# Kernel optimization log

Hardware: AMD Instinct MI355X
Metric: run time of the kernel (lower is better)

Reference implementation:

```python
import jax, jax.numpy as jnp
import numpy as np
import math

EPS = 1e-5


def _layernorm(x, gamma, beta):
    mu = jnp.mean(x, axis=-1, keepdims=True)
    var = jnp.mean(jnp.square(x - mu), axis=-1, keepdims=True)
    return (x - mu) * jax.lax.rsqrt(var + EPS) * gamma + beta


def setup_inputs() -> dict:
    key = jax.random.key(0)
    ks = jax.random.split(key, 8)
    B, Sq, Sk, D = 2, 2048, 2048, 1024
    s = 1.0 / math.sqrt(D)
    return {
        "Q": jax.random.normal(ks[0], (B, Sq, D), jnp.float32),
        "K": jax.random.normal(ks[1], (B, Sk, D), jnp.float32),
        "Wq": jax.random.normal(ks[2], (D, D), jnp.float32) * s,
        "bq": jnp.zeros((D,), jnp.float32),
        "Wk": jax.random.normal(ks[3], (D, D), jnp.float32) * s,
        "bk": jnp.zeros((D,), jnp.float32),
        "Wv": jax.random.normal(ks[4], (D, D), jnp.float32) * s,
        "bv": jnp.zeros((D,), jnp.float32),
        "Wo": jax.random.normal(ks[5], (D, D), jnp.float32) * s,
        "bo": jnp.zeros((D,), jnp.float32),
        "g0": jnp.ones((D,), jnp.float32),
        "b0": jnp.zeros((D,), jnp.float32),
        "g1": jnp.ones((D,), jnp.float32),
        "b1": jnp.zeros((D,), jnp.float32),
    }


def reference(Q, K, Wq, bq, Wk, bk, Wv, bv, Wo, bo, g0, b0, g1, b1):
    H = 16
    B, Sq, D = Q.shape
    dh = D // H
    Qp = Q @ Wq + bq                      # [B,Sq,D]
    Kp = K @ Wk + bk                      # [B,Sk,D]
    # Faithful to source: fc_v is applied to the ALREADY-projected K
    Vp = Kp @ Wv + bv                     # [B,Sk,D]
    # split heads: [B,S,H,dh] -> [B,H,S,dh]
    Qh = Qp.reshape(B, Sq, H, dh).transpose(0, 2, 1, 3)
    Kh = Kp.reshape(B, -1, H, dh).transpose(0, 2, 1, 3)
    Vh = Vp.reshape(B, -1, H, dh).transpose(0, 2, 1, 3)
    scores = jnp.einsum("bhqd,bhkd->bhqk", Qh, Kh) / math.sqrt(dh)
    attn = jax.nn.softmax(scores, axis=-1)  # dropout is identity in eval mode
    Oh = Qh + jnp.einsum("bhqk,bhkd->bhqd", attn, Vh)
    O = Oh.transpose(0, 2, 1, 3).reshape(B, Sq, D)
    O = _layernorm(O, g0, b0)
    O = O + jax.nn.gelu(O @ Wo + bo, approximate=False)
    O = _layernorm(O, g1, b1)
    return O
```

## Files before the change

kernel.cpp:

```cpp
#include <hip/hip_runtime.h>
#include <hip/hip_bf16.h>

typedef __attribute__((ext_vector_type(8))) short short8;
typedef __attribute__((ext_vector_type(4))) float f32x4;
typedef __attribute__((ext_vector_type(8))) unsigned short ushort8;

__device__ __forceinline__ unsigned short f32_to_bf16(float f) {
  return __builtin_bit_cast(unsigned short, __float2bfloat16(f));
}
__device__ __forceinline__ float bf16_to_f32(unsigned short u) {
  return __builtin_bit_cast(float, (unsigned)u << 16);
}

__device__ __forceinline__ void gload_lds16(const unsigned short* g, unsigned short* l) {
  __builtin_amdgcn_global_load_lds((const __attribute__((address_space(1))) void*)g,
                                   (__attribute__((address_space(3))) void*)l, 16, 0, 0);
}

__global__ __launch_bounds__(256) void transpose4_kernel(const float* __restrict__ W0,
                                                         const float* __restrict__ W1,
                                                         const float* __restrict__ W2,
                                                         const float* __restrict__ W3,
                                                         unsigned short* __restrict__ T0,
                                                         unsigned short* __restrict__ T1,
                                                         unsigned short* __restrict__ T2,
                                                         unsigned short* __restrict__ T3) {
  __shared__ float t[32][33];
  const int D = 1024;
  const float* Ws[4] = {W0, W1, W2, W3};
  unsigned short* Ts[4] = {T0, T1, T2, T3};
  const float* W = Ws[blockIdx.z];
  unsigned short* WT = Ts[blockIdx.z];
  int bx = blockIdx.x, by = blockIdx.y;
  int tx = threadIdx.x, ty = threadIdx.y;
#pragma unroll
  for (int i = 0; i < 4; ++i)
    t[ty * 4 + i][tx] = W[(size_t)(by * 32 + ty * 4 + i) * D + bx * 32 + tx];
  __syncthreads();
#pragma unroll
  for (int i = 0; i < 4; ++i) {
    int r = ty * 4 + i;
    WT[(size_t)(bx * 32 + r) * D + by * 32 + tx] = f32_to_bf16(t[tx][r]);
  }
}

template <bool GELU_RES, bool A_F32>
__device__ __forceinline__ void gemm_body(const void* __restrict__ Av,
                                          const unsigned short* __restrict__ Bt,
                                          const float* __restrict__ bias,
                                          const unsigned short* __restrict__ res16,
                                          float* __restrict__ out32,
                                          unsigned short* __restrict__ out16,
                                          unsigned short* __restrict__ outT,
                                          float o16_scale,
                                          int M, int N, int K,
                                          unsigned short* As, unsigned short* Bs) {
  const int tid = threadIdx.x;
  const int lane = tid & 63, wid = tid >> 6;
  const int wm = wid >> 2, wn = wid & 3;
  const int m0 = blockIdx.x * 64, n0 = blockIdx.y * 128;
  const int lr = lane & 15, lg = lane >> 4;
  const int xs = lr & 7;
  f32x4 acc[2][2] = {};
  for (int kt = 0; kt < K; kt += 64) {
#pragma unroll
    for (int i = 0; i < 2; ++i) {
      int c = tid + i * 512;
      int r = c >> 3, pc = c & 7;
      int lc = pc ^ (r & 7);
      gload_lds16(Bt + (size_t)(n0 + r) * K + kt + lc * 8, Bs + c * 8);
    }
    {
      int c = tid;
      int r = c >> 3, pc = c & 7;
      int lc = pc ^ (r & 7);
      if (A_F32) {
        const float* src = (const float*)Av + (size_t)(m0 + r) * K + kt + lc * 8;
        float4 f0 = *(const float4*)(src);
        float4 f1 = *(const float4*)(src + 4);
        ushort8 o;
        o[0] = f32_to_bf16(f0.x); o[1] = f32_to_bf16(f0.y);
        o[2] = f32_to_bf16(f0.z); o[3] = f32_to_bf16(f0.w);
        o[4] = f32_to_bf16(f1.x); o[5] = f32_to_bf16(f1.y);
        o[6] = f32_to_bf16(f1.z); o[7] = f32_to_bf16(f1.w);
        *(ushort8*)(As + c * 8) = o;
      } else {
        gload_lds16((const unsigned short*)Av + (size_t)(m0 + r) * K + kt + lc * 8,
                    As + c * 8);
      }
    }
    __syncthreads();
#pragma unroll
    for (int ks = 0; ks < 2; ++ks) {
      short8 af[2], bfr[2];
#pragma unroll
      for (int mf = 0; mf < 2; ++mf)
        af[mf] = *(const short8*)(As + (wm * 32 + mf * 16 + lr) * 64 +
                                  (((ks * 4 + lg) ^ xs) << 3));
#pragma unroll
      for (int nf = 0; nf < 2; ++nf)
        bfr[nf] = *(const short8*)(Bs + (wn * 32 + nf * 16 + lr) * 64 +
                                   (((ks * 4 + lg) ^ xs) << 3));
#pragma unroll
      for (int mf = 0; mf < 2; ++mf)
#pragma unroll
        for (int nf = 0; nf < 2; ++nf)
          acc[mf][nf] = __builtin_amdgcn_mfma_f32_16x16x32_bf16(af[mf], bfr[nf], acc[mf][nf], 0, 0, 0);
    }
    __syncthreads();
  }
#pragma unroll
  for (int nf = 0; nf < 2; ++nf) {
    int cn = n0 + wn * 32 + nf * 16 + lr;
    float bv = bias[cn];
#pragma unroll
    for (int mf = 0; mf < 2; ++mf) {
      int rm0 = m0 + wm * 32 + mf * 16 + lg * 4;
      float vv[4];
#pragma unroll
      for (int j = 0; j < 4; ++j) {
        float v = acc[mf][nf][j] + bv;
        if (GELU_RES) {
          float g = 0.5f * v * (1.0f + erff(v * 0.70710678118f));
          v = bf16_to_f32(res16[(size_t)(rm0 + j) * N + cn]) + g;
        }
        vv[j] = v;
        if (out32) out32[(size_t)(rm0 + j) * N + cn] = v;
        if (out16) out16[(size_t)(rm0 + j) * N + cn] = f32_to_bf16(v * o16_scale);
      }
      if (outT) {
        int bb = rm0 >> 11, kk = rm0 & 2047;
        int hh = cn >> 6, dd = cn & 63;
        int kin = kk & 63, kb = kk & ~63;
        int nfk = kin >> 4, lgk = (kin >> 2) & 3;
        int kperm = kb + (nfk >> 1) * 32 + lgk * 8 + (nfk & 1) * 4;
        ushort4 tv;
        tv.x = f32_to_bf16(vv[0]); tv.y = f32_to_bf16(vv[1]);
        tv.z = f32_to_bf16(vv[2]); tv.w = f32_to_bf16(vv[3]);
        *(ushort4*)(outT + ((size_t)((bb * 16 + hh) * 64 + dd)) * 2048 + kperm) = tv;
      }
    }
  }
}

template <bool GELU_RES>
__global__ __launch_bounds__(512) void gemm_kernel(const unsigned short* __restrict__ A,
                                                   const unsigned short* __restrict__ Bt,
                                                   const float* __restrict__ bias,
                                                   const unsigned short* __restrict__ res16,
                                                   float* __restrict__ out32,
                                                   unsigned short* __restrict__ out16,
                                                   unsigned short* __restrict__ outT,
                                                   int M, int N, int K) {
  __shared__ unsigned short As[64 * 64];
  __shared__ unsigned short Bs[128 * 64];
  gemm_body<GELU_RES, false>(A, Bt, bias, res16, out32, out16, outT, 1.0f, M, N, K, As, Bs);
}

__global__ __launch_bounds__(512) void gemm_qk_kernel(const float* __restrict__ A0,
                                                      const float* __restrict__ A1,
                                                      const unsigned short* __restrict__ B0,
                                                      const unsigned short* __restrict__ B1,
                                                      const float* __restrict__ bias0,
                                                      const float* __restrict__ bias1,
                                                      unsigned short* __restrict__ o16_0,
                                                      unsigned short* __restrict__ o16_1,
                                                      int M, int N, int K) {
  __shared__ unsigned short As[64 * 64];
  __shared__ unsigned short Bs[128 * 64];
  int z = blockIdx.z;
  const float SCALE2 = 0.125f * 1.44269504089f;
  gemm_body<false, true>(z ? (const void*)A1 : (const void*)A0, z ? B1 : B0,
                         z ? bias1 : bias0, nullptr,
                         nullptr, z ? o16_1 : o16_0, nullptr,
                         z ? 1.0f : SCALE2, M, N, K, As, Bs);
}

__global__ __launch_bounds__(256) void attn_kernel(const unsigned short* __restrict__ Qp,
                                                   const unsigned short* __restrict__ Kp,
                                                   const unsigned short* __restrict__ VpT,
                                                   unsigned short* __restrict__ O) {
  const int S = 2048, D = 1024;
  __shared__ unsigned short Ks[64 * 64];
  __shared__ unsigned short Vs[64 * 64];
  const int id = blockIdx.x;
  const int swz = (id & 7) * 128 + (id >> 3);
  const int bh = swz >> 5, qt = swz & 31;
  const int b = bh >> 4, h = bh & 15;
  const int tid = threadIdx.x, lane = tid & 63, w = tid >> 6;
  const int lr = lane & 15, lg = lane >> 4;
  const int xs = lr & 7;
  const size_t base = (size_t)(b * S) * D + h * 64;
  const size_t vbase = (size_t)(bh * 64) * S;
  const int q0 = qt * 64 + w * 16;
  const float INV_SCALE2 = 1.0f / (0.125f * 1.44269504089f);

  short8 qf[2];
#pragma unroll
  for (int ks = 0; ks < 2; ++ks)
    qf[ks] = *(const short8*)(Qp + base + (size_t)(q0 + lr) * D + ks * 32 + lg * 8);

  f32x4 oacc[4] = {};
  float m2 = -1e30f, lsum = 0.f;

  for (int kt = 0; kt < S; kt += 64) {
#pragma unroll
    for (int i = 0; i < 2; ++i) {
      int c = tid + i * 256;
      int r = c >> 3, pc = c & 7;
      int lc = pc ^ (r & 7);
      gload_lds16(Kp + base + (size_t)(kt + r) * D + lc * 8, Ks + c * 8);
      gload_lds16(VpT + vbase + (size_t)r * S + kt + lc * 8, Vs + c * 8);
    }
    __syncthreads();

    f32x4 sacc[4] = {};
    __builtin_amdgcn_s_setprio(1);
#pragma unroll
    for (int ks = 0; ks < 2; ++ks) {
#pragma unroll
      for (int nf = 0; nf < 4; ++nf) {
        short8 kf = *(const short8*)(Ks + (nf * 16 + lr) * 64 +
                                     (((ks * 4 + lg) ^ xs) << 3));
        sacc[nf] = __builtin_amdgcn_mfma_f32_16x16x32_bf16(kf, qf[ks], sacc[nf], 0, 0, 0);
      }
    }
    __builtin_amdgcn_s_setprio(0);

    float sm = sacc[0][0];
#pragma unroll
    for (int nf = 0; nf < 4; ++nf)
#pragma unroll
      for (int r = 0; r < 4; ++r) sm = fmaxf(sm, sacc[nf][r]);
    sm = fmaxf(sm, __shfl_xor(sm, 16));
    sm = fmaxf(sm, __shfl_xor(sm, 32));
    if (__any(sm > m2 + 8.0f)) {
      float m2n = fmaxf(m2, sm);
      float alpha = __builtin_amdgcn_exp2f(m2 - m2n);
      m2 = m2n;
      lsum *= alpha;
      float a0 = __shfl(alpha, lg * 4 + 0);
      float a1 = __shfl(alpha, lg * 4 + 1);
      float a2 = __shfl(alpha, lg * 4 + 2);
      float a3 = __shfl(alpha, lg * 4 + 3);
#pragma unroll
      for (int dblk = 0; dblk < 4; ++dblk) {
        oacc[dblk][0] *= a0; oacc[dblk][1] *= a1;
        oacc[dblk][2] *= a2; oacc[dblk][3] *= a3;
      }
    }
    float rsum = 0.f;
    short8 pf[2];
#pragma unroll
    for (int nf = 0; nf < 4; ++nf) {
      float p0 = __builtin_amdgcn_exp2f(sacc[nf][0] - m2);
      float p1 = __builtin_amdgcn_exp2f(sacc[nf][1] - m2);
      float p2 = __builtin_amdgcn_exp2f(sacc[nf][2] - m2);
      float p3 = __builtin_amdgcn_exp2f(sacc[nf][3] - m2);
      rsum += (p0 + p1) + (p2 + p3);
      int ks = nf >> 1, e0 = (nf & 1) * 4;
      pf[ks][e0 + 0] = (short)f32_to_bf16(p0);
      pf[ks][e0 + 1] = (short)f32_to_bf16(p1);
      pf[ks][e0 + 2] = (short)f32_to_bf16(p2);
      pf[ks][e0 + 3] = (short)f32_to_bf16(p3);
    }
    rsum += __shfl_xor(rsum, 16);
    rsum += __shfl_xor(rsum, 32);
    lsum += rsum;

    __builtin_amdgcn_s_setprio(1);
#pragma unroll
    for (int ks = 0; ks < 2; ++ks) {
#pragma unroll
      for (int dblk = 0; dblk < 4; ++dblk) {
        short8 vf = *(const short8*)(Vs + (dblk * 16 + lr) * 64 +
                                     (((ks * 4 + lg) ^ xs) << 3));
        oacc[dblk] = __builtin_amdgcn_mfma_f32_16x16x32_bf16(pf[ks], vf, oacc[dblk], 0, 0, 0);
      }
    }
    __builtin_amdgcn_s_setprio(0);
    __syncthreads();
  }

  float rinv = 1.0f / lsum;
  float r0 = __shfl(rinv, lg * 4 + 0);
  float r1 = __shfl(rinv, lg * 4 + 1);
  float r2 = __shfl(rinv, lg * 4 + 2);
  float r3 = __shfl(rinv, lg * 4 + 3);
#pragma unroll
  for (int dblk = 0; dblk < 4; ++dblk) {
    float rr[4] = {r0, r1, r2, r3};
#pragma unroll
    for (int j = 0; j < 4; ++j) {
      size_t idx = base + (size_t)(q0 + lg * 4 + j) * D + dblk * 16 + lr;
      float qres = bf16_to_f32(Qp[idx]) * INV_SCALE2;
      O[idx] = f32_to_bf16(qres + oacc[dblk][j] * rr[j]);
    }
  }
}

__global__ __launch_bounds__(256) void ln_bf16_kernel(const unsigned short* __restrict__ X,
                                                      const float* __restrict__ g,
                                                      const float* __restrict__ bta,
                                                      unsigned short* __restrict__ out16,
                                                      float* __restrict__ out32) {
  const int D = 1024;
  int row = blockIdx.x;
  int t = threadIdx.x;
  ushort4 xu = *(const ushort4*)(X + (size_t)row * D + t * 4);
  float4 v;
  v.x = bf16_to_f32(xu.x); v.y = bf16_to_f32(xu.y);
  v.z = bf16_to_f32(xu.z); v.w = bf16_to_f32(xu.w);
  float s = v.x + v.y + v.z + v.w;
  float s2 = v.x * v.x + v.y * v.y + v.z * v.z + v.w * v.w;
#pragma unroll
  for (int off = 1; off < 64; off <<= 1) {
    s += __shfl_xor(s, off, 64);
    s2 += __shfl_xor(s2, off, 64);
  }
  __shared__ float red[8];
  int wid = t >> 6, lane = t & 63;
  if (lane == 0) { red[wid] = s; red[4 + wid] = s2; }
  __syncthreads();
  s = red[0] + red[1] + red[2] + red[3];
  s2 = red[4] + red[5] + red[6] + red[7];
  float mu = s * (1.f / 1024.f);
  float var = s2 * (1.f / 1024.f) - mu * mu;
  float rs = rsqrtf(var + 1e-5f);
  float4 gv = *(const float4*)(g + t * 4);
  float4 bv = *(const float4*)(bta + t * 4);
  float4 o;
  o.x = (v.x - mu) * rs * gv.x + bv.x;
  o.y = (v.y - mu) * rs * gv.y + bv.y;
  o.z = (v.z - mu) * rs * gv.z + bv.z;
  o.w = (v.w - mu) * rs * gv.w + bv.w;
  if (out16) {
    ushort4 h;
    h.x = f32_to_bf16(o.x); h.y = f32_to_bf16(o.y);
    h.z = f32_to_bf16(o.z); h.w = f32_to_bf16(o.w);
    *(ushort4*)(out16 + (size_t)row * D + t * 4) = h;
  }
  if (out32) *(float4*)(out32 + (size_t)row * D + t * 4) = o;
}

extern "C" void kernel_launch(void* const* d_in, const int* in_sizes, int n_in,
                              void* d_out, int out_size, void* d_ws, size_t ws_size,
                              hipStream_t stream) {
  const float* Q = (const float*)d_in[0];
  const float* K = (const float*)d_in[1];
  const float* Wq = (const float*)d_in[2];
  const float* bq = (const float*)d_in[3];
  const float* Wk = (const float*)d_in[4];
  const float* bk = (const float*)d_in[5];
  const float* Wv = (const float*)d_in[6];
  const float* bv = (const float*)d_in[7];
  const float* Wo = (const float*)d_in[8];
  const float* bo = (const float*)d_in[9];
  const float* g0 = (const float*)d_in[10];
  const float* b0 = (const float*)d_in[11];
  const float* g1 = (const float*)d_in[12];
  const float* b1 = (const float*)d_in[13];
  float* out = (float*)d_out;

  const int M = 4096, D = 1024;
  char* p = (char*)d_ws;
  auto alloc = [&](size_t n) { char* r = p; p += (n + 255) & ~(size_t)255; return r; };
  unsigned short* WqT = (unsigned short*)alloc((size_t)D * D * 2);
  unsigned short* WkT = (unsigned short*)alloc((size_t)D * D * 2);
  unsigned short* WvT = (unsigned short*)alloc((size_t)D * D * 2);
  unsigned short* WoT = (unsigned short*)alloc((size_t)D * D * 2);
  unsigned short* Qp16 = (unsigned short*)alloc((size_t)M * D * 2);
  unsigned short* Kp16 = (unsigned short*)alloc((size_t)M * D * 2);
  unsigned short* VpT = (unsigned short*)alloc((size_t)M * D * 2);
  unsigned short* O16 = (unsigned short*)alloc((size_t)M * D * 2);
  unsigned short* O1_16 = (unsigned short*)alloc((size_t)M * D * 2);
  unsigned short* O2_16 = (unsigned short*)alloc((size_t)M * D * 2);

  transpose4_kernel<<<dim3(32, 32, 4), dim3(32, 8), 0, stream>>>(Wq, Wk, Wv, Wo,
                                                                 WqT, WkT, WvT, WoT);

  dim3 gg(M / 64, D / 128);
  gemm_qk_kernel<<<dim3(M / 64, D / 128, 2), dim3(512), 0, stream>>>(
      Q, K, WqT, WkT, bq, bk, Qp16, Kp16, M, D, D);
  gemm_kernel<false><<<gg, dim3(512), 0, stream>>>(Kp16, WvT, bv, nullptr, nullptr, nullptr,
                                                   VpT, M, D, D);

  attn_kernel<<<dim3(1024), dim3(256), 0, stream>>>(Qp16, Kp16, VpT, O16);

  ln_bf16_kernel<<<dim3(M), dim3(256), 0, stream>>>(O16, g0, b0, O1_16, nullptr);
  gemm_kernel<true><<<gg, dim3(512), 0, stream>>>(O1_16, WoT, bo, O1_16, nullptr, O2_16,
                                                  nullptr, M, D, D);
  ln_bf16_kernel<<<dim3(M), dim3(256), 0, stream>>>(O2_16, g1, b1, nullptr, out);
}
```

Measured before the change: 145.0 us.

## Split attention over key halves and merge partials in fused layernorm

Attention blocks now process half of the key sequence each, doubling the grid and writing unnormalized partial outputs along with per-row max and sum statistics. A new layernorm kernel merges the two partials with log-sum-exp weighting, adds the scaled Q residual and applies the first layernorm. This aims to raise occupancy and parallelism in the attention stage, at the cost of extra partial-output memory traffic and bf16 rounding of partials before the merge.

```diff
diff --git a/kernel.cpp b/kernel.cpp
--- a/kernel.cpp
+++ b/kernel.cpp
@@ -179,13 +179,18 @@
 __global__ __launch_bounds__(256) void attn_kernel(const unsigned short* __restrict__ Qp,
                                                    const unsigned short* __restrict__ Kp,
                                                    const unsigned short* __restrict__ VpT,
-                                                   unsigned short* __restrict__ O) {
+                                                   unsigned short* __restrict__ O0,
+                                                   unsigned short* __restrict__ O1,
+                                                   float* __restrict__ Mst,
+                                                   float* __restrict__ Lst) {
   const int S = 2048, D = 1024;
   __shared__ unsigned short Ks[64 * 64];
   __shared__ unsigned short Vs[64 * 64];
   const int id = blockIdx.x;
-  const int swz = (id & 7) * 128 + (id >> 3);
-  const int bh = swz >> 5, qt = swz & 31;
+  const int swz = (id & 7) * 256 + (id >> 3);
+  const int z = swz >> 10;
+  const int rest = swz & 1023;
+  const int bh = rest >> 5, qt = rest & 31;
   const int b = bh >> 4, h = bh & 15;
   const int tid = threadIdx.x, lane = tid & 63, w = tid >> 6;
   const int lr = lane & 15, lg = lane >> 4;
@@ -193,7 +198,6 @@
   const size_t base = (size_t)(b * S) * D + h * 64;
   const size_t vbase = (size_t)(bh * 64) * S;
   const int q0 = qt * 64 + w * 16;
-  const float INV_SCALE2 = 1.0f / (0.125f * 1.44269504089f);
 
   short8 qf[2];
 #pragma unroll
@@ -203,7 +207,8 @@
   f32x4 oacc[4] = {};
   float m2 = -1e30f, lsum = 0.f;
 
-  for (int kt = 0; kt < S; kt += 64) {
+  const int kt0 = z * 1024;
+  for (int kt = kt0; kt < kt0 + 1024; kt += 64) {
 #pragma unroll
     for (int i = 0; i < 2; ++i) {
       int c = tid + i * 256;
@@ -282,21 +287,72 @@
     __syncthreads();
   }
 
-  float rinv = 1.0f / lsum;
-  float r0 = __shfl(rinv, lg * 4 + 0);
-  float r1 = __shfl(rinv, lg * 4 + 1);
-  float r2 = __shfl(rinv, lg * 4 + 2);
-  float r3 = __shfl(rinv, lg * 4 + 3);
-#pragma unroll
-  for (int dblk = 0; dblk < 4; ++dblk) {
-    float rr[4] = {r0, r1, r2, r3};
+  unsigned short* Op = z ? O1 : O0;
+#pragma unroll
+  for (int dblk = 0; dblk < 4; ++dblk)
 #pragma unroll
     for (int j = 0; j < 4; ++j) {
       size_t idx = base + (size_t)(q0 + lg * 4 + j) * D + dblk * 16 + lr;
-      float qres = bf16_to_f32(Qp[idx]) * INV_SCALE2;
-      O[idx] = f32_to_bf16(qres + oacc[dblk][j] * rr[j]);
-    }
-  }
+      Op[idx] = f32_to_bf16(oacc[dblk][j]);
+    }
+  if (lg == 0) {
+    int row = b * 2048 + q0 + lr;
+    Mst[(size_t)z * 65536 + row * 16 + h] = m2;
+    Lst[(size_t)z * 65536 + row * 16 + h] = lsum;
+  }
+}
+
+__global__ __launch_bounds__(256) void ln_merge_kernel(const unsigned short* __restrict__ X0,
+                                                       const unsigned short* __restrict__ X1,
+                                                       const float* __restrict__ Mst,
+                                                       const float* __restrict__ Lst,
+                                                       const unsigned short* __restrict__ Qp,
+                                                       const float* __restrict__ g,
+                                                       const float* __restrict__ bta,
+                                                       unsigned short* __restrict__ out16) {
+  const int D = 1024;
+  int row = blockIdx.x;
+  int t = threadIdx.x;
+  int hh = t >> 4;
+  size_t off = (size_t)row * D + t * 4;
+  const float INV_SCALE2 = 1.0f / (0.125f * 1.44269504089f);
+  ushort4 a = *(const ushort4*)(X0 + off);
+  ushort4 bb = *(const ushort4*)(X1 + off);
+  ushort4 qr = *(const ushort4*)(Qp + off);
+  float m1 = Mst[row * 16 + hh], m2v = Mst[65536 + row * 16 + hh];
+  float l1 = Lst[row * 16 + hh], l2v = Lst[65536 + row * 16 + hh];
+  float mm = fmaxf(m1, m2v);
+  float w1 = __builtin_amdgcn_exp2f(m1 - mm), w2 = __builtin_amdgcn_exp2f(m2v - mm);
+  float rl = 1.0f / (l1 * w1 + l2v * w2);
+  float4 v;
+  v.x = bf16_to_f32(qr.x) * INV_SCALE2 + (bf16_to_f32(a.x) * w1 + bf16_to_f32(bb.x) * w2) * rl;
+  v.y = bf16_to_f32(qr.y) * INV_SCALE2 + (bf16_to_f32(a.y) * w1 + bf16_to_f32(bb.y) * w2) * rl;
+  v.z = bf16_to_f32(qr.z) * INV_SCALE2 + (bf16_to_f32(a.z) * w1 + bf16_to_f32(bb.z) * w2) * rl;
+  v.w = bf16_to_f32(qr.w) * INV_SCALE2 + (bf16_to_f32(a.w) * w1 + bf16_to_f32(bb.w) * w2) * rl;
+  float s = v.x + v.y + v.z + v.w;
+  float s2 = v.x * v.x + v.y * v.y + v.z * v.z + v.w * v.w;
+#pragma unroll
+  for (int off2 = 1; off2 < 64; off2 <<= 1) {
+    s += __shfl_xor(s, off2, 64);
+    s2 += __shfl_xor(s2, off2, 64);
+  }
+  __shared__ float red[8];
+  int wid = t >> 6, lane = t & 63;
+  if (lane == 0) { red[wid] = s; red[4 + wid] = s2; }
+  __syncthreads();
+  s = red[0] + red[1] + red[2] + red[3];
+  s2 = red[4] + red[5] + red[6] + red[7];
+  float mu = s * (1.f / 1024.f);
+  float var = s2 * (1.f / 1024.f) - mu * mu;
+  float rs = rsqrtf(var + 1e-5f);
+  float4 gv = *(const float4*)(g + t * 4);
+  float4 bv = *(const float4*)(bta + t * 4);
+  ushort4 h;
+  h.x = f32_to_bf16((v.x - mu) * rs * gv.x + bv.x);
+  h.y = f32_to_bf16((v.y - mu) * rs * gv.y + bv.y);
+  h.z = f32_to_bf16((v.z - mu) * rs * gv.z + bv.z);
+  h.w = f32_to_bf16((v.w - mu) * rs * gv.w + bv.w);
+  *(ushort4*)(out16 + off) = h;
 }
 
 __global__ __launch_bounds__(256) void ln_bf16_kernel(const unsigned short* __restrict__ X,
@@ -372,7 +428,10 @@
   unsigned short* Qp16 = (unsigned short*)alloc((size_t)M * D * 2);
   unsigned short* Kp16 = (unsigned short*)alloc((size_t)M * D * 2);
   unsigned short* VpT = (unsigned short*)alloc((size_t)M * D * 2);
-  unsigned short* O16 = (unsigned short*)alloc((size_t)M * D * 2);
+  unsigned short* O0 = (unsigned short*)alloc((size_t)M * D * 2);
+  unsigned short* O1 = (unsigned short*)alloc((size_t)M * D * 2);
+  float* Mst = (float*)alloc((size_t)2 * 65536 * 4);
+  float* Lst = (float*)alloc((size_t)2 * 65536 * 4);
   unsigned short* O1_16 = (unsigned short*)alloc((size_t)M * D * 2);
   unsigned short* O2_16 = (unsigned short*)alloc((size_t)M * D * 2);
 
@@ -385,9 +444,10 @@
   gemm_kernel<false><<<gg, dim3(512), 0, stream>>>(Kp16, WvT, bv, nullptr, nullptr, nullptr,
                                                    VpT, M, D, D);
 
-  attn_kernel<<<dim3(1024), dim3(256), 0, stream>>>(Qp16, Kp16, VpT, O16);
-
-  ln_bf16_kernel<<<dim3(M), dim3(256), 0, stream>>>(O16, g0, b0, O1_16, nullptr);
+  attn_kernel<<<dim3(2048), dim3(256), 0, stream>>>(Qp16, Kp16, VpT, O0, O1, Mst, Lst);
+
+  ln_merge_kernel<<<dim3(M), dim3(256), 0, stream>>>(O0, O1, Mst, Lst, Qp16,
+                                                     g0, b0, O1_16);
   gemm_kernel<true><<<gg, dim3(512), 0, stream>>>(O1_16, WoT, bo, O1_16, nullptr, O2_16,
                                                   nullptr, M, D, D);
   ln_bf16_kernel<<<dim3(M), dim3(256), 0, stream>>>(O2_16, g1, b1, nullptr, out);
```

After: 149.3 us. 1.03x slower.
